# Performance work log

Hardware: AMD Instinct MI355X
Metric: run time of the kernel (lower is better)

Reference implementation:

```python
import jax, jax.numpy as jnp
import numpy as np

EMB = 512
HEADS = 8

def setup_inputs() -> dict:
    key = jax.random.key(0)
    ks = jax.random.split(key, 9)
    s = 1.0 / np.sqrt(EMB)
    x = jax.random.normal(ks[0], (32, 4096, EMB), dtype=jnp.float32)
    Wq = jax.random.normal(ks[1], (EMB, EMB), dtype=jnp.float32) * s
    bq = jax.random.normal(ks[2], (EMB,), dtype=jnp.float32) * s
    Wk = jax.random.normal(ks[3], (EMB, EMB), dtype=jnp.float32) * s
    bk = jax.random.normal(ks[4], (EMB,), dtype=jnp.float32) * s
    Wv = jax.random.normal(ks[5], (EMB, EMB), dtype=jnp.float32) * s
    bv = jax.random.normal(ks[6], (EMB,), dtype=jnp.float32) * s
    Wo = jax.random.normal(ks[7], (EMB, EMB), dtype=jnp.float32) * s
    bo = jax.random.normal(ks[8], (EMB,), dtype=jnp.float32) * s
    return {"x": x, "Wq": Wq, "bq": bq, "Wk": Wk, "bk": bk,
            "Wv": Wv, "bv": bv, "Wo": Wo, "bo": bo}

def reference(x, Wq, bq, Wk, bk, Wv, bv, Wo, bo):
    b, n, e = x.shape
    h = HEADS
    d = e // h
    scale = jnp.asarray(d ** 0.5, x.dtype)
    # torch Linear: y = x @ W.T + b
    q = (x @ Wq.T + bq).reshape(b, n, h, d)
    k = (x @ Wk.T + bk).reshape(b, n, h, d)
    v = (x @ Wv.T + bv).reshape(b, n, h, d)
    # NOTE: contracts over sequence axis n (faithful to original einsum),
    # producing a (b, h, d, d) feature-feature score matrix.
    qk = jnp.einsum('bnhq,bnhk->bhqk', q, k) / scale
    attn = jax.nn.softmax(qk, axis=-1)  # softmax over head_dim axis
    # dropout is identity at inference
    weighted = jnp.einsum('bhqk,bnhk->bnhq', attn, v).reshape(b, n, e)
    return weighted @ Wo.T + bo
```

## Files before the change

kernel.cpp:

```cpp
#include <hip/hip_runtime.h>
#include <hip/hip_bf16.h>
#include <stdint.h>

#define BATCH 32
#define SEQ   4096
#define EMB   512
#define HEADS 8
#define HD    64
#define SCALE 0.125f

typedef __attribute__((ext_vector_type(8))) short bf16x8;
typedef __attribute__((ext_vector_type(4))) float f32x4;

__device__ __forceinline__ unsigned short f2bf(float f) {
    union { float f; unsigned int u; } v; v.f = f;
    unsigned int u = v.u;
    return (unsigned short)((u + 0x7FFFu + ((u >> 16) & 1u)) >> 16);
}
__device__ __forceinline__ float bf2f(unsigned short h) {
    union { unsigned int u; float f; } v; v.u = ((unsigned int)h) << 16;
    return v.f;
}
__device__ __forceinline__ unsigned int cvtpk(float lo, float hi) {
    unsigned int r;
    asm("v_cvt_pk_bf16_f32 %0, %1, %2" : "=v"(r) : "v"(lo), "v"(hi));
    return r;
}
__device__ __forceinline__ float lo_as_f(unsigned int p) {
    union { unsigned int u; float f; } v; v.u = p << 16; return v.f;
}
__device__ __forceinline__ float hi_as_f(unsigned int p) {
    union { unsigned int u; float f; } v; v.u = p & 0xFFFF0000u; return v.f;
}

#define MFMA16(a, b, c) __builtin_amdgcn_mfma_f32_16x16x32_bf16((a), (b), (c), 0, 0, 0)

union F4 { float4 v; float f[4]; };
struct Regs { F4 a0, a1, a2, a3; };

template <int NCHUNK, bool XBF>
__global__ __launch_bounds__(1024) void k1_gram(const float* __restrict__ x,
                                                float* __restrict__ P,
                                                float* __restrict__ svp,
                                                unsigned short* __restrict__ xbf) {
  constexpr int KC  = SEQ / NCHUNK;
  constexpr int NIT = KC / 32;
  constexpr int NWG = BATCH * 4 * NCHUNK;
  constexpr int PER = NWG / 8;
  const int bid = blockIdx.x;
  const int wk  = (bid & 7) * PER + (bid >> 3);
  const int c   = (NCHUNK == 2) ? (wk & 1) : 0;
  const int tt  = (NCHUNK == 2) ? ((wk >> 1) & 3) : (wk & 3);
  const int b   = (NCHUNK == 2) ? (wk >> 3) : (wk >> 2);
  const int mt = (tt >> 1) & 1, nt = tt & 1;
  const int m0 = mt * 256, n0 = nt * 256;
  const bool diag = (mt == nt);
  const float* __restrict__ xb = x + (size_t)b * SEQ * EMB;
  const int kbeg = c * KC;

  __shared__ unsigned short L[2][64 * 148];
  __shared__ float SR[256][8];

  const int tid  = threadIdx.x;
  const int lane = tid & 63;
  const int wave = tid >> 6;
  const int wr = (wave >> 2) * 64;
  const int wc = (wave & 3) * 64;
  const int er  = lane & 15;
  const int kb8 = (lane >> 4) * 8;

  const int fg   = lane;
  const int kgrp = wave >> 1;
  const bool isB = (wave & 1);
  const int pcol = isB ? n0 : m0;
  const bool active = (!diag) || (!isB);

  f32x4 acc[4][4];
#pragma unroll
  for (int i = 0; i < 4; ++i)
#pragma unroll
    for (int j = 0; j < 4; ++j) acc[i][j] = (f32x4){0.f, 0.f, 0.f, 0.f};

  float sacc[4] = {0.f, 0.f, 0.f, 0.f};

  Regs r0;

  auto loadreg = [&](int t) {
    const float* p = &xb[(size_t)(kbeg + t * 32 + kgrp * 4) * EMB + pcol + fg * 4];
    r0.a0.v = *(const float4*)p;
    r0.a1.v = *(const float4*)(p + EMB);
    r0.a2.v = *(const float4*)(p + 2 * EMB);
    r0.a3.v = *(const float4*)(p + 3 * EMB);
  };

  auto stage = [&](int t) {
    unsigned short* __restrict__ Ld = &L[isB ? 1 : 0][0];
#pragma unroll
    for (int i = 0; i < 4; ++i) {
      uint2 w;
      w.x = cvtpk(r0.a0.f[i], r0.a1.f[i]);
      w.y = cvtpk(r0.a2.f[i], r0.a3.f[i]);
      *(uint2*)&Ld[fg * 148 + i * 36 + kgrp * 4] = w;
    }
    if (diag) {
#pragma unroll
      for (int i = 0; i < 4; ++i)
        sacc[i] += (r0.a0.f[i] + r0.a1.f[i]) + (r0.a2.f[i] + r0.a3.f[i]);
      if (XBF) {
        unsigned short* xp = &xbf[((size_t)b * SEQ + kbeg + t * 32 + kgrp * 4) * EMB + m0 + fg * 4];
        uint2 xr;
        xr.x = cvtpk(r0.a0.f[0], r0.a0.f[1]); xr.y = cvtpk(r0.a0.f[2], r0.a0.f[3]);
        *(uint2*)&xp[0] = xr;
        xr.x = cvtpk(r0.a1.f[0], r0.a1.f[1]); xr.y = cvtpk(r0.a1.f[2], r0.a1.f[3]);
        *(uint2*)&xp[EMB] = xr;
        xr.x = cvtpk(r0.a2.f[0], r0.a2.f[1]); xr.y = cvtpk(r0.a2.f[2], r0.a2.f[3]);
        *(uint2*)&xp[2 * EMB] = xr;
        xr.x = cvtpk(r0.a3.f[0], r0.a3.f[1]); xr.y = cvtpk(r0.a3.f[2], r0.a3.f[3]);
        *(uint2*)&xp[3 * EMB] = xr;
      }
    }
  };

  auto frag = [&](const unsigned short* __restrict__ Ls, int e) -> bf16x8 {
    const int off = (e >> 2) * 148 + (e & 3) * 36 + kb8;
    union { bf16x8 v; uint2 u[2]; } r;
    r.u[0] = *(const uint2*)&Ls[off];
    r.u[1] = *(const uint2*)&Ls[off + 4];
    return r.v;
  };

  if (active) loadreg(0);

  for (int it = 0; it < NIT; ++it) {
    __syncthreads();
    if (active) stage(it);
    __syncthreads();
    if (active && (it + 1 < NIT)) loadreg(it + 1);

    const unsigned short* __restrict__ LAs = &L[0][0];
    const unsigned short* __restrict__ LBs = diag ? LAs : &L[1][0];
    bf16x8 bfr[4];
#pragma unroll
    for (int ns = 0; ns < 4; ++ns) bfr[ns] = frag(LBs, wc + ns * 16 + er);
    {
      bf16x8 a0f = frag(LAs, wr + er);
      bf16x8 a1f = frag(LAs, wr + 16 + er);
#pragma unroll
      for (int ns = 0; ns < 4; ++ns) {
        acc[0][ns] = MFMA16(a0f, bfr[ns], acc[0][ns]);
        acc[1][ns] = MFMA16(a1f, bfr[ns], acc[1][ns]);
      }
    }
    {
      bf16x8 a2f = frag(LAs, wr + 32 + er);
      bf16x8 a3f = frag(LAs, wr + 48 + er);
#pragma unroll
      for (int ns = 0; ns < 4; ++ns) {
        acc[2][ns] = MFMA16(a2f, bfr[ns], acc[2][ns]);
        acc[3][ns] = MFMA16(a3f, bfr[ns], acc[3][ns]);
      }
    }
  }

  float* __restrict__ Pc = P + (size_t)(c * BATCH + b) * EMB * EMB;
#pragma unroll
  for (int ms = 0; ms < 4; ++ms)
#pragma unroll
    for (int ns = 0; ns < 4; ++ns)
#pragma unroll
      for (int r = 0; r < 4; ++r) {
        const int row = m0 + wr + ms * 16 + ((lane >> 4) * 4) + r;
        const int col = n0 + wc + ns * 16 + (lane & 15);
        Pc[(size_t)row * EMB + col] = acc[ms][ns][r];
      }

  if (diag) {
    __syncthreads();
    if (!isB) {
#pragma unroll
      for (int i = 0; i < 4; ++i) SR[fg * 4 + i][kgrp] = sacc[i];
    }
    __syncthreads();
    if (tid < 256) {
      float v = 0.f;
#pragma unroll
      for (int j = 0; j < 8; ++j) v += SR[tid][j];
      svp[(size_t)(c * BATCH + b) * EMB + m0 + tid] = v;
    }
  }
}

template <bool TWO>
__global__ __launch_bounds__(256) void k2a_wqg(const float* __restrict__ Wq,
                                               const float* __restrict__ P,
                                               float* __restrict__ A) {
  const int bid = blockIdx.x;
  const int wk  = (bid & 7) * 64 + (bid >> 3);
  const int b  = wk >> 4;
  const int mt = (wk >> 2) & 3;
  const int nt = wk & 3;
  const int m0 = mt * 128, n0 = nt * 128;
  const float* __restrict__ P0b = P + (size_t)b * EMB * EMB;
  const float* __restrict__ P1b = P + (size_t)(BATCH + b) * EMB * EMB;

  __shared__ unsigned short LA[128][40];
  __shared__ unsigned short LBhi[128][40];
  __shared__ unsigned short LBlo[128][40];

  const int tid  = threadIdx.x;
  const int lane = tid & 63;
  const int wave = tid >> 6;
  const int wr = (wave >> 1) * 64;
  const int wc = (wave & 1) * 64;

  f32x4 acc[4][4];
#pragma unroll
  for (int i = 0; i < 4; ++i)
#pragma unroll
    for (int j = 0; j < 4; ++j) acc[i][j] = (f32x4){0.f, 0.f, 0.f, 0.f};

  const int rA = tid >> 3, fgA = tid & 7;

  for (int k0 = 0; k0 < EMB; k0 += 32) {
    __syncthreads();
#pragma unroll
    for (int it = 0; it < 4; ++it) {
      const int r = rA + it * 32;
      const float4 v = *(const float4*)&Wq[(size_t)(m0 + r) * EMB + k0 + fgA * 4];
      uint2 u; u.x = cvtpk(v.x, v.y); u.y = cvtpk(v.z, v.w);
      *(uint2*)&LA[r][fgA * 4] = u;
    }
#pragma unroll
    for (int it = 0; it < 4; ++it) {
      const int r = rA + it * 32;
      float4 v = *(const float4*)&P0b[(size_t)(n0 + r) * EMB + k0 + fgA * 4];
      if (TWO) {
        const float4 v1 = *(const float4*)&P1b[(size_t)(n0 + r) * EMB + k0 + fgA * 4];
        v.x += v1.x; v.y += v1.y; v.z += v1.z; v.w += v1.w;
      }
      uint2 h; h.x = cvtpk(v.x, v.y); h.y = cvtpk(v.z, v.w);
      uint2 l;
      l.x = cvtpk(v.x - lo_as_f(h.x), v.y - hi_as_f(h.x));
      l.y = cvtpk(v.z - lo_as_f(h.y), v.w - hi_as_f(h.y));
      *(uint2*)&LBhi[r][fgA * 4] = h;
      *(uint2*)&LBlo[r][fgA * 4] = l;
    }
    __syncthreads();
    bf16x8 af[4], bh[4], bl[4];
#pragma unroll
    for (int ms = 0; ms < 4; ++ms)
      af[ms] = *(const bf16x8*)&LA[wr + ms*16 + (lane & 15)][(lane >> 4) * 8];
#pragma unroll
    for (int ns = 0; ns < 4; ++ns) {
      bh[ns] = *(const bf16x8*)&LBhi[wc + ns*16 + (lane & 15)][(lane >> 4) * 8];
      bl[ns] = *(const bf16x8*)&LBlo[wc + ns*16 + (lane & 15)][(lane >> 4) * 8];
    }
#pragma unroll
    for (int ms = 0; ms < 4; ++ms)
#pragma unroll
      for (int ns = 0; ns < 4; ++ns) {
        acc[ms][ns] = MFMA16(af[ms], bh[ns], acc[ms][ns]);
        acc[ms][ns] = MFMA16(af[ms], bl[ns], acc[ms][ns]);
      }
  }

  float* __restrict__ Ab = A + (size_t)b * EMB * EMB;
#pragma unroll
  for (int ms = 0; ms < 4; ++ms)
#pragma unroll
    for (int ns = 0; ns < 4; ++ns)
#pragma unroll
      for (int r = 0; r < 4; ++r) {
        const int row = m0 + wr + ms*16 + ((lane >> 4) * 4) + r;
        const int col = n0 + wc + ns*16 + (lane & 15);
        Ab[(size_t)row * EMB + col] = acc[ms][ns][r];
      }
}

template <int NCHUNK>
__global__ __launch_bounds__(256) void k2b_logits(const float* __restrict__ A,
                                                  const float* __restrict__ Wq,
                                                  const float* __restrict__ Wk,
                                                  const float* __restrict__ bq,
                                                  const float* __restrict__ bk,
                                                  const float* __restrict__ svp,
                                                  unsigned short* __restrict__ attn) {
  const int blk = blockIdx.x;
  const int b = blk >> 3;
  const int h = blk & 7;
  const float* __restrict__ Ab = A + (size_t)b * EMB * EMB + (size_t)h * HD * EMB;

  __shared__ unsigned short LAhi[64][40];
  __shared__ unsigned short LAlo[64][40];
  __shared__ unsigned short LB[64][40];
  __shared__ float U[HD], W[HD];

  const int tid  = threadIdx.x;
  const int lane = tid & 63;
  const int wave = tid >> 6;

  if (tid < 128) {
    const int q = tid & 63;
    const float* __restrict__ wrow = (tid < 64 ? Wq : Wk) + (size_t)(h * HD + q) * EMB;
    float a = 0.f;
    for (int i = 0; i < EMB; i += 4) {
      const float4 wv = *(const float4*)&wrow[i];
      float4 sv = *(const float4*)&svp[(size_t)b * EMB + i];
      if (NCHUNK == 2) {
        const float4 s1 = *(const float4*)&svp[(size_t)(BATCH + b) * EMB + i];
        sv.x += s1.x; sv.y += s1.y; sv.z += s1.z; sv.w += s1.w;
      }
      a += wv.x*sv.x + wv.y*sv.y + wv.z*sv.z + wv.w*sv.w;
    }
    if (tid < 64) U[q] = a; else W[q] = a;
  }

  f32x4 acc[4];
#pragma unroll
  for (int i = 0; i < 4; ++i) acc[i] = (f32x4){0.f, 0.f, 0.f, 0.f};

  const int r8 = tid >> 3, fg8 = tid & 7;

  for (int k0 = 0; k0 < EMB; k0 += 32) {
    __syncthreads();
#pragma unroll
    for (int it = 0; it < 2; ++it) {
      const int r = r8 + it * 32;
      const float4 v = *(const float4*)&Ab[(size_t)r * EMB + k0 + fg8 * 4];
      uint2 h2; h2.x = cvtpk(v.x, v.y); h2.y = cvtpk(v.z, v.w);
      uint2 l2;
      l2.x = cvtpk(v.x - lo_as_f(h2.x), v.y - hi_as_f(h2.x));
      l2.y = cvtpk(v.z - lo_as_f(h2.y), v.w - hi_as_f(h2.y));
      *(ushort4*)&LAhi[r][fg8*4] = *(ushort4*)&h2;
      *(ushort4*)&LAlo[r][fg8*4] = *(ushort4*)&l2;
      const float4 wv = *(const float4*)&Wk[(size_t)(h*HD + r) * EMB + k0 + fg8 * 4];
      uint2 ub; ub.x = cvtpk(wv.x, wv.y); ub.y = cvtpk(wv.z, wv.w);
      *(ushort4*)&LB[r][fg8*4] = *(ushort4*)&ub;
    }
    __syncthreads();
    const bf16x8 ah = *(const bf16x8*)&LAhi[wave*16 + (lane & 15)][(lane >> 4) * 8];
    const bf16x8 al = *(const bf16x8*)&LAlo[wave*16 + (lane & 15)][(lane >> 4) * 8];
#pragma unroll
    for (int ns = 0; ns < 4; ++ns) {
      const bf16x8 bb = *(const bf16x8*)&LB[ns*16 + (lane & 15)][(lane >> 4) * 8];
      acc[ns] = MFMA16(ah, bb, acc[ns]);
      acc[ns] = MFMA16(al, bb, acc[ns]);
    }
  }

  const int colb = lane & 15;
  float bkv[4], wv_[4];
#pragma unroll
  for (int ns = 0; ns < 4; ++ns) {
    bkv[ns] = bk[h*HD + ns*16 + colb];
    wv_[ns] = W[ns*16 + colb];
  }
  unsigned short* __restrict__ ab = attn + (size_t)(b * HEADS + h) * HD * HD;
#pragma unroll
  for (int r = 0; r < 4; ++r) {
    const int row = wave*16 + ((lane >> 4) * 4) + r;
    const float bqv = bq[h*HD + row];
    const float uv  = U[row];
    float vals[4];
#pragma unroll
    for (int ns = 0; ns < 4; ++ns)
      vals[ns] = (acc[ns][r] + uv * bkv[ns] + bqv * wv_[ns] + 4096.f * bqv * bkv[ns]) * SCALE;
    float mx = fmaxf(fmaxf(vals[0], vals[1]), fmaxf(vals[2], vals[3]));
#pragma unroll
    for (int m = 1; m < 16; m <<= 1) mx = fmaxf(mx, __shfl_xor(mx, m));
    float sum = 0.f;
#pragma unroll
    for (int ns = 0; ns < 4; ++ns) { vals[ns] = expf(vals[ns] - mx); sum += vals[ns]; }
#pragma unroll
    for (int m = 1; m < 16; m <<= 1) sum += __shfl_xor(sum, m);
    const float inv = 1.f / sum;
#pragma unroll
    for (int ns = 0; ns < 4; ++ns)
      ab[(size_t)row * HD + ns*16 + colb] = f2bf(vals[ns] * inv);
  }
}

__global__ __launch_bounds__(256) void k3a_c(const float* __restrict__ Wo,
                                             const unsigned short* __restrict__ attn,
                                             unsigned short* __restrict__ C) {
  const int blk = blockIdx.x;
  const int b  = blk >> 5;
  const int h  = (blk >> 2) & 7;
  const int mt = blk & 3;
  const int m0 = mt * 128;

  __shared__ unsigned short LA[128][72];
  __shared__ unsigned short LB[64][72];

  const int tid  = threadIdx.x;
  const int lane = tid & 63;
  const int wave = tid >> 6;

  {
    const int r  = tid >> 4;
    const int fg = tid & 15;
#pragma unroll
    for (int it = 0; it < 8; ++it) {
      const int rr = r + it * 16;
      const float4 v = *(const float4*)&Wo[(size_t)(m0 + rr) * EMB + h*HD + fg * 4];
      uint2 u; u.x = cvtpk(v.x, v.y); u.y = cvtpk(v.z, v.w);
      *(uint2*)&LA[rr][fg * 4] = u;
    }
  }
  {
    const unsigned short* __restrict__ ab = attn + (size_t)(b * HEADS + h) * HD * HD;
#pragma unroll
    for (int it = 0; it < 16; ++it) {
      const int f  = tid + 256 * it;
      const int q  = f >> 6;
      const int kp = f & 63;
      LB[kp][q] = ab[q * HD + kp];
    }
  }
  __syncthreads();

  f32x4 acc[2][4];
#pragma unroll
  for (int i = 0; i < 2; ++i)
#pragma unroll
    for (int j = 0; j < 4; ++j) acc[i][j] = (f32x4){0.f, 0.f, 0.f, 0.f};

#pragma unroll
  for (int kk = 0; kk < 2; ++kk) {
    bf16x8 af[2], bfr[4];
#pragma unroll
    for (int ms = 0; ms < 2; ++ms)
      af[ms] = *(const bf16x8*)&LA[wave*32 + ms*16 + (lane & 15)][kk*32 + (lane >> 4) * 8];
#pragma unroll
    for (int ns = 0; ns < 4; ++ns)
      bfr[ns] = *(const bf16x8*)&LB[ns*16 + (lane & 15)][kk*32 + (lane >> 4) * 8];
#pragma unroll
    for (int ms = 0; ms < 2; ++ms)
#pragma unroll
      for (int ns = 0; ns < 4; ++ns)
        acc[ms][ns] = MFMA16(af[ms], bfr[ns], acc[ms][ns]);
  }

  unsigned short* __restrict__ Cb = C + (size_t)b * EMB * EMB;
#pragma unroll
  for (int ms = 0; ms < 2; ++ms)
#pragma unroll
    for (int ns = 0; ns < 4; ++ns)
#pragma unroll
      for (int r = 0; r < 4; ++r) {
        const int row = m0 + wave*32 + ms*16 + ((lane >> 4) * 4) + r;
        const int col = h*HD + ns*16 + (lane & 15);
        Cb[(size_t)row * EMB + col] = f2bf(acc[ms][ns][r]);
      }
}

__global__ __launch_bounds__(256) void k3b_d(const unsigned short* __restrict__ C,
                                             const float* __restrict__ Wv,
                                             const float* __restrict__ bv,
                                             const float* __restrict__ bo,
                                             unsigned short* __restrict__ D,
                                             float* __restrict__ evec) {
  const int bid = blockIdx.x;
  const int wk  = (bid & 7) * 64 + (bid >> 3);
  const int b  = wk >> 4;
  const int mt = (wk >> 2) & 3;
  const int nt = wk & 3;
  const int m0 = mt * 128, n0 = nt * 128;
  const unsigned short* __restrict__ Cb = C + (size_t)b * EMB * EMB;

  __shared__ unsigned short LA[128][40];
  __shared__ unsigned short LB[32 * 148];
  __shared__ float BV[EMB];

  const int tid  = threadIdx.x;
  const int lane = tid & 63;
  const int wave = tid >> 6;
  const int wr = (wave >> 1) * 64;
  const int wc = (wave & 1) * 64;
  const int er  = lane & 15;
  const int kb8 = (lane >> 4) * 8;

  const bool doE = (nt == 0);
  if (doE) {
    BV[tid] = bv[tid];
    BV[tid + 256] = bv[tid + 256];
  }

  f32x4 acc[4][4];
#pragma unroll
  for (int i = 0; i < 4; ++i)
#pragma unroll
    for (int j = 0; j < 4; ++j) acc[i][j] = (f32x4){0.f, 0.f, 0.f, 0.f};

  float eacc[4] = {0.f, 0.f, 0.f, 0.f};

  const int rA = tid >> 3, fgA = tid & 7;
  const int fgB = tid & 31;
  const int kgB = tid >> 5;

  for (int k0 = 0; k0 < EMB; k0 += 32) {
    __syncthreads();
    float bvr[4];
    if (doE) {
#pragma unroll
      for (int j = 0; j < 4; ++j) bvr[j] = BV[k0 + fgA * 4 + j];
    }
#pragma unroll
    for (int it = 0; it < 4; ++it) {
      const int r = rA + it * 32;
      const ushort4 c4 = *(const ushort4*)&Cb[(size_t)(m0 + r) * EMB + k0 + fgA * 4];
      *(ushort4*)&LA[r][fgA*4] = c4;
      if (doE)
        eacc[it] += bf2f(c4.x)*bvr[0] + bf2f(c4.y)*bvr[1]
                  + bf2f(c4.z)*bvr[2] + bf2f(c4.w)*bvr[3];
    }
    {
      const float* p = &Wv[(size_t)(k0 + kgB * 4) * EMB + n0 + fgB * 4];
      F4 b0, b1, b2, b3;
      b0.v = *(const float4*)p;
      b1.v = *(const float4*)(p + EMB);
      b2.v = *(const float4*)(p + 2 * EMB);
      b3.v = *(const float4*)(p + 3 * EMB);
#pragma unroll
      for (int i = 0; i < 4; ++i) {
        uint2 w;
        w.x = cvtpk(b0.f[i], b1.f[i]);
        w.y = cvtpk(b2.f[i], b3.f[i]);
        *(uint2*)&LB[fgB * 148 + i * 36 + kgB * 4] = w;
      }
    }
    __syncthreads();
    bf16x8 af[4], bfr[4];
#pragma unroll
    for (int ms = 0; ms < 4; ++ms)
      af[ms] = *(const bf16x8*)&LA[wr + ms*16 + er][kb8];
#pragma unroll
    for (int ns = 0; ns < 4; ++ns) {
      const int e = wc + ns * 16 + er;
      const int off = (e >> 2) * 148 + (e & 3) * 36 + kb8;
      union { bf16x8 v; uint2 u[2]; } r;
      r.u[0] = *(const uint2*)&LB[off];
      r.u[1] = *(const uint2*)&LB[off + 4];
      bfr[ns] = r.v;
    }
#pragma unroll
    for (int ms = 0; ms < 4; ++ms)
#pragma unroll
      for (int ns = 0; ns < 4; ++ns)
        acc[ms][ns] = MFMA16(af[ms], bfr[ns], acc[ms][ns]);
  }

  unsigned short* __restrict__ Db = D + (size_t)b * EMB * EMB;
#pragma unroll
  for (int ms = 0; ms < 4; ++ms)
#pragma unroll
    for (int ns = 0; ns < 4; ++ns)
#pragma unroll
      for (int r = 0; r < 4; ++r) {
        const int row = m0 + wr + ms*16 + ((lane >> 4) * 4) + r;
        const int col = n0 + wc + ns*16 + (lane & 15);
        Db[(size_t)row * EMB + col] = f2bf(acc[ms][ns][r]);
      }

  if (doE) {
#pragma unroll
    for (int it = 0; it < 4; ++it) {
#pragma unroll
      for (int m = 1; m < 8; m <<= 1) eacc[it] += __shfl_xor(eacc[it], m);
      if (fgA == 0) {
        const int row = m0 + rA + it * 32;
        evec[b * EMB + row] = eacc[it] + bo[row];
      }
    }
  }
}

template <bool XBF>
__global__ __launch_bounds__(1024) void k4_out(const float* __restrict__ x,
                                               const unsigned short* __restrict__ xbf,
                                               const unsigned short* __restrict__ D,
                                               const float* __restrict__ evec,
                                               float* __restrict__ out) {
  const int bid = blockIdx.x;
  const int wk  = (bid & 7) * 128 + (bid >> 3);
  const int b  = wk >> 5;
  const int mt = wk & 31;
  const int m0 = mt * 128;
  const float* __restrict__ xb = x + (size_t)b * SEQ * EMB;
  const unsigned short* __restrict__ xbb = xbf + (size_t)b * SEQ * EMB;
  const unsigned short* __restrict__ Db = D + (size_t)b * EMB * EMB;

  __shared__ unsigned short LA[128 * 40];
  __shared__ unsigned short LB[512 * 40];

  const int tid  = threadIdx.x;
  const int lane = tid & 63;
  const int wave = tid >> 6;
  const int wr = (wave >> 3) * 64;
  const int wc = (wave & 7) * 64;
  const int er  = lane & 15;
  const int kb8 = (lane >> 4) * 8;

  const int rsA = tid >> 3;
  const int kgA = tid & 7;
  const int rsB = tid >> 1;
  const int kgB = (tid & 1) * 16;

  f32x4 acc[4][4];
#pragma unroll
  for (int i = 0; i < 4; ++i)
#pragma unroll
    for (int j = 0; j < 4; ++j) acc[i][j] = (f32x4){0.f, 0.f, 0.f, 0.f};

  uint2 ua;
  F4 fa;
  uint4 ub0, ub1;

  auto loadreg = [&](int k0) {
    if (XBF) {
      ua = *(const uint2*)&xbb[(size_t)(m0 + rsA) * EMB + k0 + kgA * 4];
    } else {
      fa.v = *(const float4*)&xb[(size_t)(m0 + rsA) * EMB + k0 + kgA * 4];
    }
    ub0 = *(const uint4*)&Db[(size_t)rsB * EMB + k0 + kgB];
    ub1 = *(const uint4*)&Db[(size_t)rsB * EMB + k0 + kgB + 8];
  };

  auto stage = [&]() {
    if (XBF) {
      *(uint2*)&LA[rsA * 40 + kgA * 4] = ua;
    } else {
      uint2 w; w.x = cvtpk(fa.f[0], fa.f[1]); w.y = cvtpk(fa.f[2], fa.f[3]);
      *(uint2*)&LA[rsA * 40 + kgA * 4] = w;
    }
    *(uint4*)&LB[rsB * 40 + kgB] = ub0;
    *(uint4*)&LB[rsB * 40 + kgB + 8] = ub1;
  };

  loadreg(0);

  for (int it = 0; it < 16; ++it) {
    __syncthreads();
    stage();
    __syncthreads();
    if (it + 1 < 16) loadreg((it + 1) * 32);

    bf16x8 bfr[4];
#pragma unroll
    for (int ns = 0; ns < 4; ++ns)
      bfr[ns] = *(const bf16x8*)&LB[(wc + ns * 16 + er) * 40 + kb8];
    {
      bf16x8 a0f = *(const bf16x8*)&LA[(wr + er) * 40 + kb8];
      bf16x8 a1f = *(const bf16x8*)&LA[(wr + 16 + er) * 40 + kb8];
#pragma unroll
      for (int ns = 0; ns < 4; ++ns) {
        acc[0][ns] = MFMA16(a0f, bfr[ns], acc[0][ns]);
        acc[1][ns] = MFMA16(a1f, bfr[ns], acc[1][ns]);
      }
    }
    {
      bf16x8 a2f = *(const bf16x8*)&LA[(wr + 32 + er) * 40 + kb8];
      bf16x8 a3f = *(const bf16x8*)&LA[(wr + 48 + er) * 40 + kb8];
#pragma unroll
      for (int ns = 0; ns < 4; ++ns) {
        acc[2][ns] = MFMA16(a2f, bfr[ns], acc[2][ns]);
        acc[3][ns] = MFMA16(a3f, bfr[ns], acc[3][ns]);
      }
    }
  }

  float ev4[4];
#pragma unroll
  for (int ns = 0; ns < 4; ++ns)
    ev4[ns] = evec[b * EMB + wc + ns * 16 + (lane & 15)];

#pragma unroll
  for (int ms = 0; ms < 4; ++ms)
#pragma unroll
    for (int ns = 0; ns < 4; ++ns)
#pragma unroll
      for (int r = 0; r < 4; ++r) {
        const int row = m0 + wr + ms * 16 + ((lane >> 4) * 4) + r;
        const int col = wc + ns * 16 + (lane & 15);
        out[((size_t)b * SEQ + row) * EMB + col] = acc[ms][ns][r] + ev4[ns];
      }
}

extern "C" void kernel_launch(void* const* d_in, const int* in_sizes, int n_in,
                              void* d_out, int out_size, void* d_ws, size_t ws_size,
                              hipStream_t stream) {
  (void)in_sizes; (void)n_in; (void)out_size;
  const float* x  = (const float*)d_in[0];
  const float* Wq = (const float*)d_in[1];
  const float* bq = (const float*)d_in[2];
  const float* Wk = (const float*)d_in[3];
  const float* bk = (const float*)d_in[4];
  const float* Wv = (const float*)d_in[5];
  const float* bv = (const float*)d_in[6];
  const float* Wo = (const float*)d_in[7];
  const float* bo = (const float*)d_in[8];
  float* out = (float*)d_out;

  char* ws = (char*)d_ws;
  const size_t MB = (size_t)1 << 20;
  const size_t XBF_BYTES = (size_t)BATCH * SEQ * EMB * 2;
  const size_t NEED2 = XBF_BYTES + 98 * MB + 256 * 1024;
  const size_t NEED1 = XBF_BYTES + 66 * MB + 256 * 1024;

  if (ws_size >= NEED2) {
    unsigned short* xbf  = (unsigned short*)(ws);
    float*          P    = (float*)(ws + XBF_BYTES);
    unsigned short* Cm   = (unsigned short*)(ws + XBF_BYTES);
    unsigned short* Dm   = (unsigned short*)(ws + XBF_BYTES + 16 * MB);
    float*          A    = (float*)(ws + XBF_BYTES + 64 * MB);
    unsigned short* attn = (unsigned short*)(ws + XBF_BYTES + 96 * MB);
    float*          svp  = (float*)(ws + XBF_BYTES + 98 * MB);
    float*          ev   = (float*)(ws + XBF_BYTES + 98 * MB + 192 * 1024);

    hipLaunchKernelGGL((k1_gram<2, true>), dim3(BATCH * 8),  dim3(1024), 0, stream, x, P, svp, xbf);
    hipLaunchKernelGGL((k2a_wqg<true>),    dim3(BATCH * 16), dim3(256), 0, stream, Wq, P, A);
    hipLaunchKernelGGL((k2b_logits<2>),    dim3(BATCH * 8),  dim3(256), 0, stream, A, Wq, Wk, bq, bk, svp, attn);
    hipLaunchKernelGGL(k3a_c,              dim3(BATCH * 32), dim3(256), 0, stream, Wo, attn, Cm);
    hipLaunchKernelGGL(k3b_d,              dim3(BATCH * 16), dim3(256), 0, stream, Cm, Wv, bv, bo, Dm, ev);
    hipLaunchKernelGGL((k4_out<true>),     dim3(BATCH * 32), dim3(1024), 0, stream, x, xbf, Dm, ev, out);
  } else if (ws_size >= NEED1) {
    unsigned short* xbf  = (unsigned short*)(ws);
    float*          P    = (float*)(ws + XBF_BYTES);
    unsigned short* Cm   = (unsigned short*)(ws + XBF_BYTES);
    unsigned short* Dm   = (unsigned short*)(ws + XBF_BYTES + 16 * MB);
    float*          A    = (float*)(ws + XBF_BYTES + 32 * MB);
    unsigned short* attn = (unsigned short*)(ws + XBF_BYTES + 64 * MB);
    float*          svp  = (float*)(ws + XBF_BYTES + 66 * MB);
    float*          ev   = (float*)(ws + XBF_BYTES + 66 * MB + 192 * 1024);

    hipLaunchKernelGGL((k1_gram<1, true>), dim3(BATCH * 4),  dim3(1024), 0, stream, x, P, svp, xbf);
    hipLaunchKernelGGL((k2a_wqg<false>),   dim3(BATCH * 16), dim3(256), 0, stream, Wq, P, A);
    hipLaunchKernelGGL((k2b_logits<1>),    dim3(BATCH * 8),  dim3(256), 0, stream, A, Wq, Wk, bq, bk, svp, attn);
    hipLaunchKernelGGL(k3a_c,              dim3(BATCH * 32), dim3(256), 0, stream, Wo, attn, Cm);
    hipLaunchKernelGGL(k3b_d,              dim3(BATCH * 16), dim3(256), 0, stream, Cm, Wv, bv, bo, Dm, ev);
    hipLaunchKernelGGL((k4_out<true>),     dim3(BATCH * 32), dim3(1024), 0, stream, x, xbf, Dm, ev, out);
  } else {
    unsigned short* xbf  = (unsigned short*)(ws);
    float*          P    = (float*)(ws);
    unsigned short* Cm   = (unsigned short*)(ws);
    unsigned short* Dm   = (unsigned short*)(ws + 16 * MB);
    float*          A    = (float*)(ws + 32 * MB);
    unsigned short* attn = (unsigned short*)(ws + 64 * MB);
    float*          svp  = (float*)(ws + 66 * MB);
    float*          ev   = (float*)(ws + 66 * MB + 192 * 1024);

    hipLaunchKernelGGL((k1_gram<1, false>), dim3(BATCH * 4),  dim3(1024), 0, stream, x, P, svp, xbf);
    hipLaunchKernelGGL((k2a_wqg<false>),    dim3(BATCH * 16), dim3(256), 0, stream, Wq, P, A);
    hipLaunchKernelGGL((k2b_logits<1>),     dim3(BATCH * 8),  dim3(256), 0, stream, A, Wq, Wk, bq, bk, svp, attn);
    hipLaunchKernelGGL(k3a_c,               dim3(BATCH * 32), dim3(256), 0, stream, Wo, attn, Cm);
    hipLaunchKernelGGL(k3b_d,               dim3(BATCH * 16), dim3(256), 0, stream, Cm, Wv, bv, bo, Dm, ev);
    hipLaunchKernelGGL((k4_out<false>),     dim3(BATCH * 32), dim3(1024), 0, stream, x, xbf, Dm, ev, out);
  }
}
```

Baseline: 361.4 us.

## Prefetch next K-tile global loads into registers during MFMA compute

```diff
diff --git a/kernel.cpp b/kernel.cpp
--- a/kernel.cpp
+++ b/kernel.cpp
@@ -221,31 +221,44 @@
 
   const int rA = tid >> 3, fgA = tid & 7;
 
-  for (int k0 = 0; k0 < EMB; k0 += 32) {
-    __syncthreads();
+  F4 ra[4], rb0[4], rb1[4];
+
+  auto loadreg = [&](int k0) {
 #pragma unroll
     for (int it = 0; it < 4; ++it) {
       const int r = rA + it * 32;
-      const float4 v = *(const float4*)&Wq[(size_t)(m0 + r) * EMB + k0 + fgA * 4];
-      uint2 u; u.x = cvtpk(v.x, v.y); u.y = cvtpk(v.z, v.w);
-      *(uint2*)&LA[r][fgA * 4] = u;
-    }
+      ra[it].v  = *(const float4*)&Wq[(size_t)(m0 + r) * EMB + k0 + fgA * 4];
+      rb0[it].v = *(const float4*)&P0b[(size_t)(n0 + r) * EMB + k0 + fgA * 4];
+      if (TWO)
+        rb1[it].v = *(const float4*)&P1b[(size_t)(n0 + r) * EMB + k0 + fgA * 4];
+    }
+  };
+
+  auto stage = [&]() {
 #pragma unroll
     for (int it = 0; it < 4; ++it) {
       const int r = rA + it * 32;
-      float4 v = *(const float4*)&P0b[(size_t)(n0 + r) * EMB + k0 + fgA * 4];
-      if (TWO) {
-        const float4 v1 = *(const float4*)&P1b[(size_t)(n0 + r) * EMB + k0 + fgA * 4];
-        v.x += v1.x; v.y += v1.y; v.z += v1.z; v.w += v1.w;
-      }
-      uint2 h; h.x = cvtpk(v.x, v.y); h.y = cvtpk(v.z, v.w);
+      uint2 u; u.x = cvtpk(ra[it].f[0], ra[it].f[1]); u.y = cvtpk(ra[it].f[2], ra[it].f[3]);
+      *(uint2*)&LA[r][fgA * 4] = u;
+      float v0 = rb0[it].f[0], v1 = rb0[it].f[1], v2 = rb0[it].f[2], v3 = rb0[it].f[3];
+      if (TWO) { v0 += rb1[it].f[0]; v1 += rb1[it].f[1]; v2 += rb1[it].f[2]; v3 += rb1[it].f[3]; }
+      uint2 h; h.x = cvtpk(v0, v1); h.y = cvtpk(v2, v3);
       uint2 l;
-      l.x = cvtpk(v.x - lo_as_f(h.x), v.y - hi_as_f(h.x));
-      l.y = cvtpk(v.z - lo_as_f(h.y), v.w - hi_as_f(h.y));
+      l.x = cvtpk(v0 - lo_as_f(h.x), v1 - hi_as_f(h.x));
+      l.y = cvtpk(v2 - lo_as_f(h.y), v3 - hi_as_f(h.y));
       *(uint2*)&LBhi[r][fgA * 4] = h;
       *(uint2*)&LBlo[r][fgA * 4] = l;
     }
-    __syncthreads();
+  };
+
+  loadreg(0);
+
+  for (int k0 = 0; k0 < EMB; k0 += 32) {
+    __syncthreads();
+    stage();
+    __syncthreads();
+    if (k0 + 32 < EMB) loadreg(k0 + 32);
+
     bf16x8 af[4], bh[4], bl[4];
 #pragma unroll
     for (int ms = 0; ms < 4; ++ms)
@@ -299,6 +312,36 @@
   const int lane = tid & 63;
   const int wave = tid >> 6;
 
+  const int r8 = tid >> 3, fg8 = tid & 7;
+
+  F4 va[2], vw[2];
+
+  auto loadreg = [&](int k0) {
+#pragma unroll
+    for (int it = 0; it < 2; ++it) {
+      const int r = r8 + it * 32;
+      va[it].v = *(const float4*)&Ab[(size_t)r * EMB + k0 + fg8 * 4];
+      vw[it].v = *(const float4*)&Wk[(size_t)(h*HD + r) * EMB + k0 + fg8 * 4];
+    }
+  };
+
+  auto stage = [&]() {
+#pragma unroll
+    for (int it = 0; it < 2; ++it) {
+      const int r = r8 + it * 32;
+      uint2 h2; h2.x = cvtpk(va[it].f[0], va[it].f[1]); h2.y = cvtpk(va[it].f[2], va[it].f[3]);
+      uint2 l2;
+      l2.x = cvtpk(va[it].f[0] - lo_as_f(h2.x), va[it].f[1] - hi_as_f(h2.x));
+      l2.y = cvtpk(va[it].f[2] - lo_as_f(h2.y), va[it].f[3] - hi_as_f(h2.y));
+      *(uint2*)&LAhi[r][fg8*4] = h2;
+      *(uint2*)&LAlo[r][fg8*4] = l2;
+      uint2 ub; ub.x = cvtpk(vw[it].f[0], vw[it].f[1]); ub.y = cvtpk(vw[it].f[2], vw[it].f[3]);
+      *(uint2*)&LB[r][fg8*4] = ub;
+    }
+  };
+
+  loadreg(0);
+
   if (tid < 128) {
     const int q = tid & 63;
     const float* __restrict__ wrow = (tid < 64 ? Wq : Wk) + (size_t)(h * HD + q) * EMB;
@@ -319,25 +362,12 @@
 #pragma unroll
   for (int i = 0; i < 4; ++i) acc[i] = (f32x4){0.f, 0.f, 0.f, 0.f};
 
-  const int r8 = tid >> 3, fg8 = tid & 7;
-
   for (int k0 = 0; k0 < EMB; k0 += 32) {
     __syncthreads();
-#pragma unroll
-    for (int it = 0; it < 2; ++it) {
-      const int r = r8 + it * 32;
-      const float4 v = *(const float4*)&Ab[(size_t)r * EMB + k0 + fg8 * 4];
-      uint2 h2; h2.x = cvtpk(v.x, v.y); h2.y = cvtpk(v.z, v.w);
-      uint2 l2;
-      l2.x = cvtpk(v.x - lo_as_f(h2.x), v.y - hi_as_f(h2.x));
-      l2.y = cvtpk(v.z - lo_as_f(h2.y), v.w - hi_as_f(h2.y));
-      *(ushort4*)&LAhi[r][fg8*4] = *(ushort4*)&h2;
-      *(ushort4*)&LAlo[r][fg8*4] = *(ushort4*)&l2;
-      const float4 wv = *(const float4*)&Wk[(size_t)(h*HD + r) * EMB + k0 + fg8 * 4];
-      uint2 ub; ub.x = cvtpk(wv.x, wv.y); ub.y = cvtpk(wv.z, wv.w);
-      *(ushort4*)&LB[r][fg8*4] = *(ushort4*)&ub;
-    }
-    __syncthreads();
+    stage();
+    __syncthreads();
+    if (k0 + 32 < EMB) loadreg(k0 + 32);
+
     const bf16x8 ah = *(const bf16x8*)&LAhi[wave*16 + (lane & 15)][(lane >> 4) * 8];
     const bf16x8 al = *(const bf16x8*)&LAlo[wave*16 + (lane & 15)][(lane >> 4) * 8];
 #pragma unroll
@@ -498,8 +528,23 @@
   const int fgB = tid & 31;
   const int kgB = tid >> 5;
 
-  for (int k0 = 0; k0 < EMB; k0 += 32) {
-    __syncthreads();
+  ushort4 rc[4];
+  F4 rb0, rb1, rb2, rb3;
+
+  auto loadreg = [&](int k0) {
+#pragma unroll
+    for (int it = 0; it < 4; ++it) {
+      const int r = rA + it * 32;
+      rc[it] = *(const ushort4*)&Cb[(size_t)(m0 + r) * EMB + k0 + fgA * 4];
+    }
+    const float* p = &Wv[(size_t)(k0 + kgB * 4) * EMB + n0 + fgB * 4];
+    rb0.v = *(const float4*)p;
+    rb1.v = *(const float4*)(p + EMB);
+    rb2.v = *(const float4*)(p + 2 * EMB);
+    rb3.v = *(const float4*)(p + 3 * EMB);
+  };
+
+  auto stage = [&](int k0) {
     float bvr[4];
     if (doE) {
 #pragma unroll
@@ -508,28 +553,28 @@
 #pragma unroll
     for (int it = 0; it < 4; ++it) {
       const int r = rA + it * 32;
-      const ushort4 c4 = *(const ushort4*)&Cb[(size_t)(m0 + r) * EMB + k0 + fgA * 4];
-      *(ushort4*)&LA[r][fgA*4] = c4;
+      *(ushort4*)&LA[r][fgA*4] = rc[it];
       if (doE)
-        eacc[it] += bf2f(c4.x)*bvr[0] + bf2f(c4.y)*bvr[1]
-                  + bf2f(c4.z)*bvr[2] + bf2f(c4.w)*bvr[3];
-    }
-    {
-      const float* p = &Wv[(size_t)(k0 + kgB * 4) * EMB + n0 + fgB * 4];
-      F4 b0, b1, b2, b3;
-      b0.v = *(const float4*)p;
-      b1.v = *(const float4*)(p + EMB);
-      b2.v = *(const float4*)(p + 2 * EMB);
-      b3.v = *(const float4*)(p + 3 * EMB);
-#pragma unroll
-      for (int i = 0; i < 4; ++i) {
-        uint2 w;
-        w.x = cvtpk(b0.f[i], b1.f[i]);
-        w.y = cvtpk(b2.f[i], b3.f[i]);
-        *(uint2*)&LB[fgB * 148 + i * 36 + kgB * 4] = w;
-      }
-    }
-    __syncthreads();
+        eacc[it] += bf2f(rc[it].x)*bvr[0] + bf2f(rc[it].y)*bvr[1]
+                  + bf2f(rc[it].z)*bvr[2] + bf2f(rc[it].w)*bvr[3];
+    }
+#pragma unroll
+    for (int i = 0; i < 4; ++i) {
+      uint2 w;
+      w.x = cvtpk(rb0.f[i], rb1.f[i]);
+      w.y = cvtpk(rb2.f[i], rb3.f[i]);
+      *(uint2*)&LB[fgB * 148 + i * 36 + kgB * 4] = w;
+    }
+  };
+
+  loadreg(0);
+
+  for (int k0 = 0; k0 < EMB; k0 += 32) {
+    __syncthreads();
+    stage(k0);
+    __syncthreads();
+    if (k0 + 32 < EMB) loadreg(k0 + 32);
+
     bf16x8 af[4], bfr[4];
 #pragma unroll
     for (int ms = 0; ms < 4; ++ms)
```

Result: faster. 347.7 us, median of 2 (-3.8%).
